# Kernel optimization log

Measured on AMD Instinct MI355X. Metric: run time of the kernel, lower is better.

## Reference

```python
import jax, jax.numpy as jnp
import numpy as np

IN_F = 1024
OUT_F = 1024
N_ORDER = 13  # grid_size=10 + spline_order=3
RMS_EPS = 1e-6


def setup_inputs() -> dict:
    key = jax.random.key(0)
    k_x, k_b, k_p = jax.random.split(key, 3)
    x = jax.random.normal(k_x, (4, 2048, IN_F), dtype=jnp.float32)
    # flax param init: normal(stddev=scale_base/sqrt(in_features)) etc.
    base_weight = jax.random.normal(k_b, (IN_F, OUT_F), dtype=jnp.float32) * (1.0 / np.sqrt(IN_F))
    poly_weight = jax.random.normal(k_p, (N_ORDER, IN_F, OUT_F), dtype=jnp.float32) * (0.1 / np.sqrt(IN_F * N_ORDER))
    rms_scale = jnp.ones((OUT_F,), dtype=jnp.float32)  # nn.RMSNorm default scale init
    return {"x": x, "base_weight": base_weight, "poly_weight": poly_weight, "rms_scale": rms_scale}


def reference(x, base_weight, poly_weight, rms_scale):
    orig_dtype = x.dtype
    prefix = x.shape[:-1]
    x_2d = x.reshape(-1, IN_F)  # [B, in]

    # Base path: SiLU(x) @ W_base in bf16
    x_c = x_2d.astype(jnp.bfloat16)
    out = jax.nn.silu(x_c) @ base_weight.astype(jnp.bfloat16)  # [B, out] bf16

    # Chebyshev recursion on tanh-normalized fp32 input
    x_safe = jnp.tanh(x_2d.astype(jnp.float32))
    pw = poly_weight.astype(jnp.bfloat16)
    T_prev = jnp.ones_like(x_safe)
    T_curr = x_safe
    out = out + T_prev.astype(jnp.bfloat16) @ pw[0]
    out = out + T_curr.astype(jnp.bfloat16) @ pw[1]
    for k in range(2, N_ORDER):  # fixed small unroll (13 orders)
        T_next = 2.0 * x_safe * T_curr - T_prev
        out = out + T_next.astype(jnp.bfloat16) @ pw[k]
        T_prev = T_curr
        T_curr = T_next

    # RMSNorm (flax default: eps=1e-6, learned scale)
    o32 = out.astype(jnp.float32)
    ms = jnp.mean(o32 * o32, axis=-1, keepdims=True)
    o32 = o32 * jax.lax.rsqrt(ms + RMS_EPS) * rms_scale
    return o32.astype(orig_dtype).reshape(prefix + (OUT_F,))
```

## Files before the change

### kernel.cpp

```cpp
#include <hip/hip_runtime.h>
#include <cstdint>

#define IN_F  1024
#define OUT_F 1024
#define NORD  13
#define BROWS 8192

typedef __bf16 bf16x8 __attribute__((ext_vector_type(8)));
typedef float  f32x4  __attribute__((ext_vector_type(4)));
typedef unsigned short u16x8 __attribute__((ext_vector_type(8)));
typedef unsigned short u16x4 __attribute__((ext_vector_type(4)));

__device__ __forceinline__ unsigned short f2bf(float f) {
  unsigned int u = __float_as_uint(f);
  unsigned int r = u + 0x7FFFu + ((u >> 16) & 1u);
  return (unsigned short)(r >> 16);
}
__device__ __forceinline__ float bf2f(unsigned short h) {
  return __uint_as_float(((unsigned int)h) << 16);
}
__device__ __forceinline__ float bfround(float f) { return bf2f(f2bf(f)); }

__device__ __forceinline__ void gload_lds16(const void* g, void* l) {
  __builtin_amdgcn_global_load_lds(
      (__attribute__((address_space(1))) unsigned int*)(uintptr_t)g,
      (__attribute__((address_space(3))) unsigned int*)(unsigned int)(uintptr_t)l,
      16, 0, 0);
}

__global__ __launch_bounds__(256)
void act_kernel(const float* __restrict__ x, unsigned short* __restrict__ A,
                int b0, int nb, int Kp) {
  int t   = threadIdx.x;
  int row = blockIdx.x * 2 + (t >> 7);
  int f0  = (t & 127) * 8;
  const float* xr = x + (size_t)row * IN_F + f0;
  float xv[8];
  *(float4*)&xv[0] = *(const float4*)&xr[0];
  *(float4*)&xv[4] = *(const float4*)&xr[4];
  unsigned short* Ar = A + (size_t)row * Kp;
  int omax = b0 + nb - 1;
  if (b0 == 0) {
    u16x8 sv;
#pragma unroll
    for (int i = 0; i < 8; i++) {
      float xc = bfround(xv[i]);
      float sg = bfround(1.0f / (1.0f + expf(-xc)));
      sv[i] = f2bf(xc * sg);
    }
    *(u16x8*)&Ar[f0] = sv;
  }
  float xs[8], tp[8], tc[8];
#pragma unroll
  for (int i = 0; i < 8; i++) { xs[i] = tanhf(xv[i]); tp[i] = 1.0f; tc[i] = xs[i]; }
  for (int o = 1; o <= omax; o++) {
    if (o >= b0) {
      int bb = o - b0;
      u16x8 sv;
#pragma unroll
      for (int i = 0; i < 8; i++) sv[i] = f2bf(tc[i]);
      *(u16x8*)&Ar[(size_t)bb * 1024 + f0] = sv;
    }
    {
#pragma clang fp contract(off)
#pragma unroll
      for (int i = 0; i < 8; i++) {
        float tm = 2.0f * xs[i] * tc[i];
        float tn = tm - tp[i];
        tp[i] = tc[i]; tc[i] = tn;
      }
    }
  }
}

__global__ __launch_bounds__(256)
void wprep_kernel(const float* __restrict__ baseW, const float* __restrict__ poly,
                  unsigned short* __restrict__ Wt, int b0, int Kp) {
  __shared__ float tile[64][65];
  int bb = blockIdx.z;
  int g  = b0 + bb;
  const float* src = (g == 0) ? baseW : (poly + (size_t)g * (IN_F * OUT_F));
  int n0 = blockIdx.x * 64, f0 = blockIdx.y * 64;
  int tx = threadIdx.x, ty = threadIdx.y;
#pragma unroll
  for (int i = 0; i < 16; i++)
    tile[ty + i * 4][tx] = src[(size_t)(f0 + ty + i * 4) * OUT_F + n0 + tx];
  __syncthreads();
#pragma unroll
  for (int i = 0; i < 16; i++)
    Wt[(size_t)(n0 + ty + i * 4) * Kp + (size_t)bb * 1024 + f0 + tx] = f2bf(tile[tx][ty + i * 4]);
}

__global__ __launch_bounds__(256)
void bias1_kernel(const float* __restrict__ pw0, float* __restrict__ partial) {
  int t  = threadIdx.x;
  int n  = blockIdx.x * 256 + t;
  int fc = blockIdx.y;
  float s = 0.f;
  for (int f = fc * 128; f < fc * 128 + 128; f++)
    s += bf2f(f2bf(pw0[(size_t)f * OUT_F + n]));
  partial[(size_t)fc * OUT_F + n] = s;
}
__global__ __launch_bounds__(256)
void bias2_kernel(const float* __restrict__ partial, float* __restrict__ bias) {
  int n = blockIdx.x * 256 + threadIdx.x;
  float s = 0.f;
#pragma unroll
  for (int fc = 0; fc < 8; fc++) s += partial[(size_t)fc * OUT_F + n];
  bias[n] = s;
}

__global__ __launch_bounds__(256, 2)
void gemm_kernel(const unsigned short* __restrict__ A, const unsigned short* __restrict__ Wt,
                 unsigned short* __restrict__ outAcc, const float* __restrict__ bias,
                 int Kp, int isFirst) {
  __shared__ unsigned short sA[128 * 64];
  __shared__ unsigned short sB[128 * 64];
  int t    = threadIdx.x;
  int m0   = blockIdx.x * 128;
  int n0   = blockIdx.y * 128;
  int wave = t >> 6, lane = t & 63;
  int lr   = lane & 15, quad = lane >> 4;
  int wm   = (wave & 1) * 64, wn = (wave >> 1) * 64;

  int rs = t >> 3;
  int jg = (t & 7) ^ (rs & 7);
  const unsigned short* aSrc = A  + (size_t)(m0 + rs) * Kp + jg * 8;
  const unsigned short* bSrc = Wt + (size_t)(n0 + rs) * Kp + jg * 8;
  char* sAc = (char*)sA;
  char* sBc = (char*)sB;
  int ldsOff = t * 16;

  int aOff[4][2], bOff[4][2];
#pragma unroll
  for (int mi = 0; mi < 4; mi++) {
    int row = wm + mi * 16 + lr;
#pragma unroll
    for (int ks = 0; ks < 2; ks++) {
      int j = ks * 4 + quad;
      aOff[mi][ks] = row * 128 + ((j ^ (row & 7)) * 16);
    }
  }
#pragma unroll
  for (int ni = 0; ni < 4; ni++) {
    int row = wn + ni * 16 + lr;
#pragma unroll
    for (int ks = 0; ks < 2; ks++) {
      int j = ks * 4 + quad;
      bOff[ni][ks] = row * 128 + ((j ^ (row & 7)) * 16);
    }
  }

  f32x4 s[4][4];
  float bsr[4];
  if (isFirst) {
#pragma unroll
    for (int ni = 0; ni < 4; ni++) bsr[ni] = bfround(bias[n0 + wn + ni * 16 + lr]);
  } else {
#pragma unroll
    for (int ni = 0; ni < 4; ni++) {
      int gn = n0 + wn + ni * 16 + lr;
#pragma unroll
      for (int mi = 0; mi < 4; mi++) {
        int gmBase = m0 + wm + mi * 16 + quad * 4;
#pragma unroll
        for (int r = 0; r < 4; r++)
          s[mi][ni][r] = bf2f(outAcc[(size_t)(gmBase + r) * OUT_F + gn]);
      }
    }
  }

  int nBlk = Kp >> 10;
  for (int blk = 0; blk < nBlk; blk++) {
    f32x4 acc[4][4];
#pragma unroll
    for (int mi = 0; mi < 4; mi++)
#pragma unroll
      for (int ni = 0; ni < 4; ni++)
        acc[mi][ni] = (f32x4){0.f, 0.f, 0.f, 0.f};

    for (int kt = 0; kt < 16; kt++) {
      __syncthreads();
      const unsigned short* aP = aSrc + blk * 1024 + kt * 64;
      const unsigned short* bP = bSrc + blk * 1024 + kt * 64;
#pragma unroll
      for (int rd = 0; rd < 4; rd++)
        gload_lds16(aP + (size_t)rd * 32 * Kp, sAc + ldsOff + rd * 4096);
#pragma unroll
      for (int rd = 0; rd < 4; rd++)
        gload_lds16(bP + (size_t)rd * 32 * Kp, sBc + ldsOff + rd * 4096);
      __syncthreads();
#pragma unroll
      for (int ks = 0; ks < 2; ks++) {
        bf16x8 af[4], bfr[4];
#pragma unroll
        for (int mi = 0; mi < 4; mi++) af[mi] = *(const bf16x8*)(sAc + aOff[mi][ks]);
#pragma unroll
        for (int ni = 0; ni < 4; ni++) bfr[ni] = *(const bf16x8*)(sBc + bOff[ni][ks]);
#pragma unroll
        for (int mi = 0; mi < 4; mi++)
#pragma unroll
          for (int ni = 0; ni < 4; ni++)
            acc[mi][ni] = __builtin_amdgcn_mfma_f32_16x16x32_bf16(af[mi], bfr[ni], acc[mi][ni], 0, 0, 0);
      }
    }

    bool firstBlk = (isFirst && blk == 0);
    if (firstBlk) {
#pragma unroll
      for (int mi = 0; mi < 4; mi++)
#pragma unroll
        for (int ni = 0; ni < 4; ni++)
#pragma unroll
          for (int r = 0; r < 4; r++) {
            float p = bfround(acc[mi][ni][r]);
            s[mi][ni][r] = bfround(p + bsr[ni]);
          }
    } else {
#pragma unroll
      for (int mi = 0; mi < 4; mi++)
#pragma unroll
        for (int ni = 0; ni < 4; ni++)
#pragma unroll
          for (int r = 0; r < 4; r++)
            s[mi][ni][r] = bfround(s[mi][ni][r] + bfround(acc[mi][ni][r]));
    }
  }

#pragma unroll
  for (int ni = 0; ni < 4; ni++) {
    int gn = n0 + wn + ni * 16 + lr;
#pragma unroll
    for (int mi = 0; mi < 4; mi++) {
      int gmBase = m0 + wm + mi * 16 + quad * 4;
#pragma unroll
      for (int r = 0; r < 4; r++)
        outAcc[(size_t)(gmBase + r) * OUT_F + gn] = f2bf(s[mi][ni][r]);
    }
  }
}

__global__ __launch_bounds__(256)
void rms_kernel(const unsigned short* __restrict__ outAcc, const float* __restrict__ scale,
                float* __restrict__ out) {
  int row = blockIdx.x;
  int t   = threadIdx.x;
  const unsigned short* src = outAcc + (size_t)row * OUT_F;
  u16x4 hv = *(const u16x4*)&src[t * 4];
  float v[4];
#pragma unroll
  for (int i = 0; i < 4; i++) v[i] = bf2f(hv[i]);
  float s = v[0]*v[0] + v[1]*v[1] + v[2]*v[2] + v[3]*v[3];
#pragma unroll
  for (int off = 32; off > 0; off >>= 1) s += __shfl_down(s, off, 64);
  __shared__ float red[4];
  if ((t & 63) == 0) red[t >> 6] = s;
  __syncthreads();
  float tot = red[0] + red[1] + red[2] + red[3];
  float sc = 1.0f / sqrtf(tot * (1.0f / OUT_F) + 1e-6f);
  float4 so = *(const float4*)&scale[t * 4];
  float4 o;
  o.x = v[0] * sc * so.x; o.y = v[1] * sc * so.y;
  o.z = v[2] * sc * so.z; o.w = v[3] * sc * so.w;
  *(float4*)&out[(size_t)row * OUT_F + t * 4] = o;
}

extern "C" void kernel_launch(void* const* d_in, const int* in_sizes, int n_in,
                              void* d_out, int out_size, void* d_ws, size_t ws_size,
                              hipStream_t stream) {
  const float* x     = (const float*)d_in[0];
  const float* baseW = (const float*)d_in[1];
  const float* poly  = (const float*)d_in[2];
  const float* scale = (const float*)d_in[3];
  float* out = (float*)d_out;

  char* ws = (char*)d_ws;
  unsigned short* outAcc = (unsigned short*)ws;
  float* bias    = (float*)(ws + 16777216);
  float* partial = (float*)(ws + 16777216 + 4096);
  size_t fixed   = 16777216 + 4096 + 32768;

  int CHB = 1;
  for (int c = NORD; c >= 1; c--) {
    size_t need = fixed + (size_t)c * 1024 * OUT_F * 2
                + (size_t)BROWS * c * 1024 * 2;
    if (need <= ws_size) { CHB = c; break; }
  }
  unsigned short* Wt = (unsigned short*)(ws + fixed);
  unsigned short* Ap = (unsigned short*)(ws + fixed + (size_t)CHB * 1024 * OUT_F * 2);

  bias1_kernel<<<dim3(4, 8), 256, 0, stream>>>(poly, partial);
  bias2_kernel<<<4, 256, 0, stream>>>(partial, bias);

  for (int b0 = 0; b0 < NORD; b0 += CHB) {
    int nb = (CHB < NORD - b0) ? CHB : (NORD - b0);
    int Kp = nb * 1024;
    act_kernel<<<BROWS / 2, 256, 0, stream>>>(x, Ap, b0, nb, Kp);
    wprep_kernel<<<dim3(16, 16, nb), dim3(64, 4), 0, stream>>>(baseW, poly, Wt, b0, Kp);
    gemm_kernel<<<dim3(BROWS / 128, 8), 256, 0, stream>>>(Ap, Wt, outAcc, bias, Kp, (b0 == 0) ? 1 : 0);
  }
  rms_kernel<<<BROWS, 256, 0, stream>>>(outAcc, scale, out);
}
```

Measured before the change: 452.8 us.

## Double-buffer LDS tiles to prefetch the next K-tile during MFMA compute

Shared-memory A and B tiles are doubled, and the next 64-wide K slice is issued with global_load_lds into the alternate buffer before the MFMAs run on the current one. One barrier per K-step replaces the two used before, so global-to-LDS latency can overlap compute and the prefetch continues across 1024-wide K blocks. LDS use per workgroup doubles to 64 KB, which may limit occupancy. The compiler may also insert conservative waits on the async loads, which would cancel the overlap.

```diff
diff --git a/kernel.cpp b/kernel.cpp
--- a/kernel.cpp
+++ b/kernel.cpp
@@ -114,8 +114,8 @@
 void gemm_kernel(const unsigned short* __restrict__ A, const unsigned short* __restrict__ Wt,
                  unsigned short* __restrict__ outAcc, const float* __restrict__ bias,
                  int Kp, int isFirst) {
-  __shared__ unsigned short sA[128 * 64];
-  __shared__ unsigned short sB[128 * 64];
+  __shared__ unsigned short sA[2][128 * 64];
+  __shared__ unsigned short sB[2][128 * 64];
   int t    = threadIdx.x;
   int m0   = blockIdx.x * 128;
   int n0   = blockIdx.y * 128;
@@ -170,7 +170,25 @@
     }
   }
 
+  int nKt  = Kp >> 6;
   int nBlk = Kp >> 10;
+
+  auto stage = [&](int gkt, int buf) {
+    const unsigned short* aP = aSrc + gkt * 64;
+    const unsigned short* bP = bSrc + gkt * 64;
+    char* dA = sAc + buf * 16384 + ldsOff;
+    char* dB = sBc + buf * 16384 + ldsOff;
+#pragma unroll
+    for (int rd = 0; rd < 4; rd++)
+      gload_lds16(aP + (size_t)rd * 32 * Kp, dA + rd * 4096);
+#pragma unroll
+    for (int rd = 0; rd < 4; rd++)
+      gload_lds16(bP + (size_t)rd * 32 * Kp, dB + rd * 4096);
+  };
+
+  stage(0, 0);
+
+  int gkt = 0;
   for (int blk = 0; blk < nBlk; blk++) {
     f32x4 acc[4][4];
 #pragma unroll
@@ -179,24 +197,20 @@
       for (int ni = 0; ni < 4; ni++)
         acc[mi][ni] = (f32x4){0.f, 0.f, 0.f, 0.f};
 
-    for (int kt = 0; kt < 16; kt++) {
+    for (int kt = 0; kt < 16; kt++, gkt++) {
       __syncthreads();
-      const unsigned short* aP = aSrc + blk * 1024 + kt * 64;
-      const unsigned short* bP = bSrc + blk * 1024 + kt * 64;
-#pragma unroll
-      for (int rd = 0; rd < 4; rd++)
-        gload_lds16(aP + (size_t)rd * 32 * Kp, sAc + ldsOff + rd * 4096);
-#pragma unroll
-      for (int rd = 0; rd < 4; rd++)
-        gload_lds16(bP + (size_t)rd * 32 * Kp, sBc + ldsOff + rd * 4096);
-      __syncthreads();
+      int nxt = gkt + 1;
+      if (nxt < nKt) stage(nxt, nxt & 1);
+      int buf = gkt & 1;
+      char* bA = sAc + buf * 16384;
+      char* bB = sBc + buf * 16384;
 #pragma unroll
       for (int ks = 0; ks < 2; ks++) {
         bf16x8 af[4], bfr[4];
 #pragma unroll
-        for (int mi = 0; mi < 4; mi++) af[mi] = *(const bf16x8*)(sAc + aOff[mi][ks]);
-#pragma unroll
-        for (int ni = 0; ni < 4; ni++) bfr[ni] = *(const bf16x8*)(sBc + bOff[ni][ks]);
+        for (int mi = 0; mi < 4; mi++) af[mi] = *(const bf16x8*)(bA + aOff[mi][ks]);
+#pragma unroll
+        for (int ni = 0; ni < 4; ni++) bfr[ni] = *(const bf16x8*)(bB + bOff[ni][ks]);
 #pragma unroll
         for (int mi = 0; mi < 4; mi++)
 #pragma unroll
```

Measured after the change: 405.5 us. 10.4% less time.
